# Kernel optimization log

Measured on AMD Instinct MI355X. Metric: run time of the kernel, lower is better.

Reference implementation:

```python
import jax, jax.numpy as jnp
import numpy as np

N_NODES = 50000
N_EDGES = 1600000
D_EDGE = 32
D_NODE = 32
D_HID = 128
D_OUT = 32


def setup_inputs() -> dict:
    key = jax.random.key(0)
    ks = jax.random.split(key, 8)
    edge_feats = jax.random.normal(ks[0], (N_EDGES, D_EDGE), dtype=jnp.float32)
    node_feats = jax.random.normal(ks[1], (N_NODES, D_NODE), dtype=jnp.float32)
    senders = jax.random.randint(ks[2], (N_EDGES,), 0, N_NODES, dtype=jnp.int64 if jax.config.jax_enable_x64 else jnp.int32)
    receivers = jax.random.randint(ks[3], (N_EDGES,), 0, N_NODES, dtype=jnp.int64 if jax.config.jax_enable_x64 else jnp.int32)
    d_in = D_EDGE + 2 * D_NODE  # 96
    W1 = jax.random.normal(ks[4], (d_in, D_HID), dtype=jnp.float32) / jnp.sqrt(jnp.float32(d_in))
    b1 = jnp.zeros((D_HID,), dtype=jnp.float32)
    W2 = jax.random.normal(ks[5], (D_HID, D_OUT), dtype=jnp.float32) / jnp.sqrt(jnp.float32(D_HID))
    b2 = jnp.zeros((D_OUT,), dtype=jnp.float32)
    return {"edge_feats": edge_feats, "node_feats": node_feats, "senders": senders,
            "receivers": receivers, "W1": W1, "b1": b1, "W2": W2, "b2": b2}


def reference(edge_feats, node_feats, senders, receivers, W1, b1, W2, b2):
    # Gather node feats to edges (target=0 -> senders, target=1 -> receivers),
    # concat with edge feats along feature dim, then edge MLP.
    sender_feats = node_feats[senders]        # [E, D_NODE]
    receiver_feats = node_feats[receivers]    # [E, D_NODE]
    collected = jnp.concatenate([edge_feats, sender_feats, receiver_feats], axis=1)  # [E, 96]
    h = jax.nn.relu(collected @ W1 + b1)      # [E, 128]
    updated_edges = h @ W2 + b2               # [E, 32]
    return updated_edges
```

## Files before the change

kernel.cpp:

```cpp
#include <hip/hip_runtime.h>

typedef __attribute__((ext_vector_type(8))) short bf16x8;
typedef __attribute__((ext_vector_type(4))) float f32x4;
typedef unsigned short ushort_t;
typedef unsigned int uint32;

#define TILE 64
#define N_EDGES 1600000
#define NT (N_EDGES / TILE)
#define GRID 768

#define CSTR 104
#define HSTR 136
#define WBUF (16 * HSTR)
#define W1_OFF (4 * WBUF)
#define W2_OFF (W1_OFF + 128 * CSTR)
#define SMEM_USHORTS (W2_OFF + 32 * HSTR)

__device__ __forceinline__ ushort_t f2bf(float x) {
    uint32 u = __builtin_bit_cast(uint32, x);
    u += 0x7FFFu + ((u >> 16) & 1u);
    return (ushort_t)(u >> 16);
}
__device__ __forceinline__ uint32 pack2(float a, float b) {
    return (uint32)f2bf(a) | ((uint32)f2bf(b) << 16);
}
__device__ __forceinline__ void store_bf16x8(ushort_t* dst, f32x4 a, f32x4 b) {
    uint4 p;
    p.x = pack2(a[0], a[1]);
    p.y = pack2(a[2], a[3]);
    p.z = pack2(b[0], b[1]);
    p.w = pack2(b[2], b[3]);
    *reinterpret_cast<uint4*>(dst) = p;
}

__global__ __launch_bounds__(256, 3)
void edge_mlp_kernel(const float* __restrict__ edge_feats,
                     const float* __restrict__ node_feats,
                     const int* __restrict__ senders,
                     const int* __restrict__ receivers,
                     const float* __restrict__ W1,
                     const float* __restrict__ b1,
                     const float* __restrict__ W2,
                     const float* __restrict__ b2,
                     float* __restrict__ out)
{
    __shared__ __align__(16) ushort_t smem[SMEM_USHORTS];
    ushort_t* w1t = smem + W1_OFF;
    ushort_t* w2t = smem + W2_OFF;

    const int tid = threadIdx.x;
    const int l   = tid & 63;
    const int llo = l & 15;
    const int lhi = l >> 4;
    const int w   = tid >> 6;
    const int r   = l >> 2;
    const int q   = l & 3;

    ushort_t* buf = smem + w * WBUF;

    for (int idx = tid; idx < 96 * 128; idx += 256) {
        int k = idx >> 7, n = idx & 127;
        w1t[n * CSTR + k] = f2bf(W1[idx]);
    }
    for (int idx = tid; idx < 128 * 32; idx += 256) {
        int n = idx >> 5, o = idx & 31;
        w2t[o * HSTR + n] = f2bf(W2[idx]);
    }

    f32x4 b1v[8], b2v[2];
#pragma unroll
    for (int ni = 0; ni < 8; ++ni)
        b1v[ni] = *reinterpret_cast<const f32x4*>(b1 + ni * 16 + lhi * 4);
#pragma unroll
    for (int oi = 0; oi < 2; ++oi)
        b2v[oi] = *reinterpret_cast<const f32x4*>(b2 + oi * 16 + lhi * 4);

    __syncthreads();

    const long stride = gridDim.x;
    const long last = (long)NT - 1;
    long t = blockIdx.x;

    long eS = t * TILE + w * 16 + r;
    int si_c = senders[eS], ri_c = receivers[eS];
    f32x4 ea, eb, sa, sb, ra, rb;
    {
        const f32x4* efp = reinterpret_cast<const f32x4*>(edge_feats + eS * 32) + q * 2;
        ea = efp[0]; eb = efp[1];
        const f32x4* sp = reinterpret_cast<const f32x4*>(node_feats + (long)si_c * 32) + q * 2;
        sa = sp[0]; sb = sp[1];
        const f32x4* rp = reinterpret_cast<const f32x4*>(node_feats + (long)ri_c * 32) + q * 2;
        ra = rp[0]; rb = rp[1];
    }
    long ts1 = t + stride; ts1 = ts1 <= last ? ts1 : last;
    long eS1 = ts1 * TILE + w * 16 + r;
    int si_n = senders[eS1], ri_n = receivers[eS1];

    for (; t < NT; t += stride) {
        ushort_t* cw = buf + r * CSTR + q * 8;
        store_bf16x8(cw,      ea, eb);
        store_bf16x8(cw + 32, sa, sb);
        store_bf16x8(cw + 64, ra, rb);

        long tn = t + stride; tn = tn <= last ? tn : last;
        f32x4 nea, neb, nsa, nsb, nra, nrb;
        {
            long eN = tn * TILE + w * 16 + r;
            const f32x4* efp = reinterpret_cast<const f32x4*>(edge_feats + eN * 32) + q * 2;
            nea = efp[0]; neb = efp[1];
            const f32x4* sp = reinterpret_cast<const f32x4*>(node_feats + (long)si_n * 32) + q * 2;
            nsa = sp[0]; nsb = sp[1];
            const f32x4* rp = reinterpret_cast<const f32x4*>(node_feats + (long)ri_n * 32) + q * 2;
            nra = rp[0]; nrb = rp[1];
        }
        long tn2 = t + 2 * stride; tn2 = tn2 <= last ? tn2 : last;
        long eN2 = tn2 * TILE + w * 16 + r;
        int si_2 = senders[eN2], ri_2 = receivers[eN2];

        f32x4 acc1[8];
#pragma unroll
        for (int ni = 0; ni < 8; ++ni) acc1[ni] = f32x4{0.f, 0.f, 0.f, 0.f};
        const ushort_t* crow = buf + llo * CSTR + lhi * 8;
        const ushort_t* w1r  = w1t + llo * CSTR + lhi * 8;
        __builtin_amdgcn_s_setprio(1);
#pragma unroll
        for (int kk = 0; kk < 3; ++kk) {
            bf16x8 bfrag = *reinterpret_cast<const bf16x8*>(crow + kk * 32);
#pragma unroll
            for (int ni = 0; ni < 8; ++ni) {
                bf16x8 afrag = *reinterpret_cast<const bf16x8*>(w1r + ni * 16 * CSTR + kk * 32);
                acc1[ni] = __builtin_amdgcn_mfma_f32_16x16x32_bf16(afrag, bfrag, acc1[ni], 0, 0, 0);
            }
        }
        __builtin_amdgcn_s_setprio(0);

#pragma unroll
        for (int ni = 0; ni < 8; ++ni) {
            float h0 = fmaxf(acc1[ni][0] + b1v[ni][0], 0.f);
            float h1 = fmaxf(acc1[ni][1] + b1v[ni][1], 0.f);
            float h2 = fmaxf(acc1[ni][2] + b1v[ni][2], 0.f);
            float h3 = fmaxf(acc1[ni][3] + b1v[ni][3], 0.f);
            uint2 p;
            p.x = pack2(h0, h1);
            p.y = pack2(h2, h3);
            *reinterpret_cast<uint2*>(buf + llo * HSTR + ni * 16 + lhi * 4) = p;
        }

        f32x4 acc2[2];
        acc2[0] = f32x4{0.f, 0.f, 0.f, 0.f};
        acc2[1] = f32x4{0.f, 0.f, 0.f, 0.f};
        const ushort_t* hrow = buf + llo * HSTR + lhi * 8;
        const ushort_t* w2r  = w2t + llo * HSTR + lhi * 8;
        __builtin_amdgcn_s_setprio(1);
#pragma unroll
        for (int kk = 0; kk < 4; ++kk) {
            bf16x8 bfrag = *reinterpret_cast<const bf16x8*>(hrow + kk * 32);
#pragma unroll
            for (int oi = 0; oi < 2; ++oi) {
                bf16x8 afrag = *reinterpret_cast<const bf16x8*>(w2r + oi * 16 * HSTR + kk * 32);
                acc2[oi] = __builtin_amdgcn_mfma_f32_16x16x32_bf16(afrag, bfrag, acc2[oi], 0, 0, 0);
            }
        }
        __builtin_amdgcn_s_setprio(0);

        float* orow = out + (t * TILE + w * 16 + llo) * 32 + lhi * 4;
#pragma unroll
        for (int oi = 0; oi < 2; ++oi) {
            f32x4 rr;
            rr[0] = acc2[oi][0] + b2v[oi][0];
            rr[1] = acc2[oi][1] + b2v[oi][1];
            rr[2] = acc2[oi][2] + b2v[oi][2];
            rr[3] = acc2[oi][3] + b2v[oi][3];
            *reinterpret_cast<f32x4*>(orow + oi * 16) = rr;
        }

        ea = nea; eb = neb; sa = nsa; sb = nsb; ra = nra; rb = nrb;
        si_n = si_2; ri_n = ri_2;
    }
}

extern "C" void kernel_launch(void* const* d_in, const int* in_sizes, int n_in,
                              void* d_out, int out_size, void* d_ws, size_t ws_size,
                              hipStream_t stream) {
    const float* edge_feats = (const float*)d_in[0];
    const float* node_feats = (const float*)d_in[1];
    const int*   senders    = (const int*)d_in[2];
    const int*   receivers  = (const int*)d_in[3];
    const float* W1         = (const float*)d_in[4];
    const float* b1         = (const float*)d_in[5];
    const float* W2         = (const float*)d_in[6];
    const float* b2         = (const float*)d_in[7];
    float* out = (float*)d_out;

    dim3 grid(GRID), block(256);
    hipLaunchKernelGGL(edge_mlp_kernel, grid, block, 0, stream,
                       edge_feats, node_feats, senders, receivers, W1, b1, W2, b2, out);
}
```

Measured before the change: 388.4 us.

## Keep MLP weight fragments in registers and alias LDS staging onto weight area

Weights are converted to bf16 in LDS once, then every wave loads its W1 and W2 MFMA A-fragments into registers. This removes per-tile LDS reads of the weights in the inner loops, and the per-wave staging buffers now reuse the weight LDS region after a barrier. Biases are folded into the accumulator initialisation instead of being added afterwards, and the prefetch registers are reused in place. Launch bounds drop to 2 waves-per-SIMD and the grid shrinks to 512 to allow the extra register pressure, which lowers occupancy and leaves less latency hiding for the random node gathers.

```diff
diff --git a/kernel.cpp b/kernel.cpp
--- a/kernel.cpp
+++ b/kernel.cpp
@@ -8,14 +8,15 @@
 #define TILE 64
 #define N_EDGES 1600000
 #define NT (N_EDGES / TILE)
-#define GRID 768
+#define GRID 512
 
 #define CSTR 104
 #define HSTR 136
+#define W1_US (128 * CSTR)
+#define W2_US (32 * HSTR)
+#define WEIGHT_US (W1_US + W2_US)
 #define WBUF (16 * HSTR)
-#define W1_OFF (4 * WBUF)
-#define W2_OFF (W1_OFF + 128 * CSTR)
-#define SMEM_USHORTS (W2_OFF + 32 * HSTR)
+#define SMEM_USHORTS WEIGHT_US
 
 __device__ __forceinline__ ushort_t f2bf(float x) {
     uint32 u = __builtin_bit_cast(uint32, x);
@@ -34,7 +35,7 @@
     *reinterpret_cast<uint4*>(dst) = p;
 }
 
-__global__ __launch_bounds__(256, 3)
+__global__ __launch_bounds__(256, 2)
 void edge_mlp_kernel(const float* __restrict__ edge_feats,
                      const float* __restrict__ node_feats,
                      const int* __restrict__ senders,
@@ -46,8 +47,6 @@
                      float* __restrict__ out)
 {
     __shared__ __align__(16) ushort_t smem[SMEM_USHORTS];
-    ushort_t* w1t = smem + W1_OFF;
-    ushort_t* w2t = smem + W2_OFF;
 
     const int tid = threadIdx.x;
     const int l   = tid & 63;
@@ -57,16 +56,34 @@
     const int r   = l >> 2;
     const int q   = l & 3;
 
-    ushort_t* buf = smem + w * WBUF;
-
-    for (int idx = tid; idx < 96 * 128; idx += 256) {
-        int k = idx >> 7, n = idx & 127;
-        w1t[n * CSTR + k] = f2bf(W1[idx]);
+    {
+        ushort_t* w1t = smem;
+        ushort_t* w2t = smem + W1_US;
+        for (int idx = tid; idx < 96 * 128; idx += 256) {
+            int k = idx >> 7, n = idx & 127;
+            w1t[n * CSTR + k] = f2bf(W1[idx]);
+        }
+        for (int idx = tid; idx < 128 * 32; idx += 256) {
+            int n = idx >> 5, o = idx & 31;
+            w2t[o * HSTR + n] = f2bf(W2[idx]);
+        }
     }
-    for (int idx = tid; idx < 128 * 32; idx += 256) {
-        int n = idx >> 5, o = idx & 31;
-        w2t[o * HSTR + n] = f2bf(W2[idx]);
-    }
+    __syncthreads();
+
+    bf16x8 w1f[8][3];
+#pragma unroll
+    for (int ni = 0; ni < 8; ++ni)
+#pragma unroll
+        for (int kk = 0; kk < 3; ++kk)
+            w1f[ni][kk] = *reinterpret_cast<const bf16x8*>(
+                smem + (ni * 16 + llo) * CSTR + kk * 32 + lhi * 8);
+    bf16x8 w2f[2][4];
+#pragma unroll
+    for (int oi = 0; oi < 2; ++oi)
+#pragma unroll
+        for (int kk = 0; kk < 4; ++kk)
+            w2f[oi][kk] = *reinterpret_cast<const bf16x8*>(
+                smem + W1_US + (oi * 16 + llo) * HSTR + kk * 32 + lhi * 8);
 
     f32x4 b1v[8], b2v[2];
 #pragma unroll
@@ -77,6 +94,8 @@
         b2v[oi] = *reinterpret_cast<const f32x4*>(b2 + oi * 16 + lhi * 4);
 
     __syncthreads();
+
+    ushort_t* buf = smem + w * WBUF;
 
     const long stride = gridDim.x;
     const long last = (long)NT - 1;
@@ -104,43 +123,39 @@
         store_bf16x8(cw + 64, ra, rb);
 
         long tn = t + stride; tn = tn <= last ? tn : last;
-        f32x4 nea, neb, nsa, nsb, nra, nrb;
         {
             long eN = tn * TILE + w * 16 + r;
             const f32x4* efp = reinterpret_cast<const f32x4*>(edge_feats + eN * 32) + q * 2;
-            nea = efp[0]; neb = efp[1];
+            ea = efp[0]; eb = efp[1];
             const f32x4* sp = reinterpret_cast<const f32x4*>(node_feats + (long)si_n * 32) + q * 2;
-            nsa = sp[0]; nsb = sp[1];
+            sa = sp[0]; sb = sp[1];
             const f32x4* rp = reinterpret_cast<const f32x4*>(node_feats + (long)ri_n * 32) + q * 2;
-            nra = rp[0]; nrb = rp[1];
+            ra = rp[0]; rb = rp[1];
         }
         long tn2 = t + 2 * stride; tn2 = tn2 <= last ? tn2 : last;
         long eN2 = tn2 * TILE + w * 16 + r;
-        int si_2 = senders[eN2], ri_2 = receivers[eN2];
+        si_n = senders[eN2]; ri_n = receivers[eN2];
 
         f32x4 acc1[8];
 #pragma unroll
-        for (int ni = 0; ni < 8; ++ni) acc1[ni] = f32x4{0.f, 0.f, 0.f, 0.f};
+        for (int ni = 0; ni < 8; ++ni) acc1[ni] = b1v[ni];
         const ushort_t* crow = buf + llo * CSTR + lhi * 8;
-        const ushort_t* w1r  = w1t + llo * CSTR + lhi * 8;
         __builtin_amdgcn_s_setprio(1);
 #pragma unroll
         for (int kk = 0; kk < 3; ++kk) {
             bf16x8 bfrag = *reinterpret_cast<const bf16x8*>(crow + kk * 32);
 #pragma unroll
-            for (int ni = 0; ni < 8; ++ni) {
-                bf16x8 afrag = *reinterpret_cast<const bf16x8*>(w1r + ni * 16 * CSTR + kk * 32);
-                acc1[ni] = __builtin_amdgcn_mfma_f32_16x16x32_bf16(afrag, bfrag, acc1[ni], 0, 0, 0);
-            }
+            for (int ni = 0; ni < 8; ++ni)
+                acc1[ni] = __builtin_amdgcn_mfma_f32_16x16x32_bf16(w1f[ni][kk], bfrag, acc1[ni], 0, 0, 0);
         }
         __builtin_amdgcn_s_setprio(0);
 
 #pragma unroll
         for (int ni = 0; ni < 8; ++ni) {
-            float h0 = fmaxf(acc1[ni][0] + b1v[ni][0], 0.f);
-            float h1 = fmaxf(acc1[ni][1] + b1v[ni][1], 0.f);
-            float h2 = fmaxf(acc1[ni][2] + b1v[ni][2], 0.f);
-            float h3 = fmaxf(acc1[ni][3] + b1v[ni][3], 0.f);
+            float h0 = fmaxf(acc1[ni][0], 0.f);
+            float h1 = fmaxf(acc1[ni][1], 0.f);
+            float h2 = fmaxf(acc1[ni][2], 0.f);
+            float h3 = fmaxf(acc1[ni][3], 0.f);
             uint2 p;
             p.x = pack2(h0, h1);
             p.y = pack2(h2, h3);
@@ -148,35 +163,22 @@
         }
 
         f32x4 acc2[2];
-        acc2[0] = f32x4{0.f, 0.f, 0.f, 0.f};
-        acc2[1] = f32x4{0.f, 0.f, 0.f, 0.f};
+        acc2[0] = b2v[0];
+        acc2[1] = b2v[1];
         const ushort_t* hrow = buf + llo * HSTR + lhi * 8;
-        const ushort_t* w2r  = w2t + llo * HSTR + lhi * 8;
         __builtin_amdgcn_s_setprio(1);
 #pragma unroll
         for (int kk = 0; kk < 4; ++kk) {
             bf16x8 bfrag = *reinterpret_cast<const bf16x8*>(hrow + kk * 32);
 #pragma unroll
-            for (int oi = 0; oi < 2; ++oi) {
-                bf16x8 afrag = *reinterpret_cast<const bf16x8*>(w2r + oi * 16 * HSTR + kk * 32);
-                acc2[oi] = __builtin_amdgcn_mfma_f32_16x16x32_bf16(afrag, bfrag, acc2[oi], 0, 0, 0);
-            }
+            for (int oi = 0; oi < 2; ++oi)
+                acc2[oi] = __builtin_amdgcn_mfma_f32_16x16x32_bf16(w2f[oi][kk], bfrag, acc2[oi], 0, 0, 0);
         }
         __builtin_amdgcn_s_setprio(0);
 
         float* orow = out + (t * TILE + w * 16 + llo) * 32 + lhi * 4;
-#pragma unroll
-        for (int oi = 0; oi < 2; ++oi) {
-            f32x4 rr;
-            rr[0] = acc2[oi][0] + b2v[oi][0];
-            rr[1] = acc2[oi][1] + b2v[oi][1];
-            rr[2] = acc2[oi][2] + b2v[oi][2];
-            rr[3] = acc2[oi][3] + b2v[oi][3];
-            *reinterpret_cast<f32x4*>(orow + oi * 16) = rr;
-        }
-
-        ea = nea; eb = neb; sa = nsa; sb = nsb; ra = nra; rb = nrb;
-        si_n = si_2; ri_n = ri_2;
+        *reinterpret_cast<f32x4*>(orow)      = acc2[0];
+        *reinterpret_cast<f32x4*>(orow + 16) = acc2[1];
     }
 }
 
```

After: 381.8 us. Within noise of the previous version (-1.7%).
